# Kernel optimization log

Measured on AMD Instinct MI355X. Metric: run time of the kernel, lower is better.

## Reference

```python
import jax, jax.numpy as jnp
import numpy as np

B, N, D, H, L = 2, 2048, 128, 8, 3
V = 32          # NUM_ATOM_TYPES (assumed)
DH = D // H
SCALE = 1.0 / (DH ** 0.5)
NEG = -1e9      # stands in for -inf in the additive attention mask
EPS = 1e-5


def _ln(x, g, b):
    m = x.mean(-1, keepdims=True)
    v = ((x - m) ** 2).mean(-1, keepdims=True)
    return (x - m) / jnp.sqrt(v + EPS) * g + b


def setup_inputs() -> dict:
    key = jax.random.key(0)
    ks = jax.random.split(key, 24)
    nrm = lambda k, shape, std=0.02: jax.random.normal(k, shape, jnp.float32) * std
    atom_embed = nrm(ks[0], (V, D)).at[0].set(0.0)  # padding_idx = 0
    cons_embed = nrm(ks[1], (1, 1, D))
    in_w = nrm(ks[2], (D, D)); in_b = jnp.zeros((D,), jnp.float32)
    qkv_w = nrm(ks[3], (L, 3 * D, D)); qkv_b = jnp.zeros((L, 3 * D), jnp.float32)
    out_w = nrm(ks[4], (L, D, D)); out_b = jnp.zeros((L, D), jnp.float32)
    ln1_g = jnp.ones((L, D), jnp.float32); ln1_b = jnp.zeros((L, D), jnp.float32)
    ln2_g = jnp.ones((L, D), jnp.float32); ln2_b = jnp.zeros((L, D), jnp.float32)
    ff1_w = nrm(ks[5], (L, 4 * D, D)); ff1_b = jnp.zeros((L, 4 * D), jnp.float32)
    ff2_w = nrm(ks[6], (L, D, 4 * D)); ff2_b = jnp.zeros((L, D), jnp.float32)
    struct_bias = nrm(ks[7], (L,), 0.5)  # scalar per layer (init 0 in torch; randomized to exercise the path)
    head_ln_g = jnp.ones((D,), jnp.float32); head_ln_b = jnp.zeros((D,), jnp.float32)
    head_w = nrm(ks[8], (1, D)); head_b = jnp.zeros((1,), jnp.float32)
    is_atom = jax.random.bernoulli(ks[9], 0.5, (B, N))
    atom_id = jax.random.randint(ks[10], (B, N), 0, V)
    mask = jax.random.bernoulli(ks[11], 0.9, (B, N))
    adjacency = (jax.random.uniform(ks[12], (B, N, N)) < 0.002).astype(jnp.float32)
    adjacency = jnp.maximum(adjacency, jnp.eye(N, dtype=jnp.float32)[None])  # self-loops
    root_idx = jax.random.randint(ks[13], (B,), 0, N)
    return dict(atom_embed=atom_embed, cons_embed=cons_embed, in_w=in_w, in_b=in_b,
                qkv_w=qkv_w, qkv_b=qkv_b, out_w=out_w, out_b=out_b,
                ln1_g=ln1_g, ln1_b=ln1_b, ln2_g=ln2_g, ln2_b=ln2_b,
                ff1_w=ff1_w, ff1_b=ff1_b, ff2_w=ff2_w, ff2_b=ff2_b,
                struct_bias=struct_bias, head_ln_g=head_ln_g, head_ln_b=head_ln_b,
                head_w=head_w, head_b=head_b, adjacency=adjacency,
                is_atom=is_atom, atom_id=atom_id, mask=mask, root_idx=root_idx)


def reference(atom_embed, cons_embed, in_w, in_b, qkv_w, qkv_b, out_w, out_b,
              ln1_g, ln1_b, ln2_g, ln2_b, ff1_w, ff1_b, ff2_w, ff2_b,
              struct_bias, head_ln_g, head_ln_b, head_w, head_b,
              adjacency, is_atom, atom_id, mask, root_idx):
    # node embeddings
    ae = atom_embed[jnp.clip(atom_id, 0, V - 1)]                     # [B,N,D]
    h = jnp.where(is_atom[..., None], ae, jnp.broadcast_to(cons_embed, (B, N, D)))
    h = h @ in_w.T + in_b
    # additive attention mask: valid pairs OK; invalid query rows attend only to self
    pair_ok = mask[:, :, None] & mask[:, None, :]
    eye = jnp.eye(N, dtype=bool)[None]
    ok = pair_ok | ((~mask)[:, :, None] & eye)
    am = jnp.where(ok, 0.0, NEG).astype(jnp.float32)                 # [B,N,N]
    for i in range(L):
        x = _ln(h, ln1_g[i], ln1_b[i])
        qkv = (x @ qkv_w[i].T + qkv_b[i]).reshape(B, N, 3, H, DH)
        q, k, v = (jnp.transpose(qkv[:, :, j], (0, 2, 1, 3)) for j in range(3))  # [B,H,N,DH]
        scores = jnp.einsum('bhqd,bhkd->bhqk', q, k) * SCALE \
                 + struct_bias[i] * adjacency[:, None] + am[:, None]
        attn = jax.nn.softmax(scores, axis=-1)
        o = jnp.einsum('bhqk,bhkd->bhqd', attn, v)
        o = jnp.transpose(o, (0, 2, 1, 3)).reshape(B, N, D)
        h = h + (o @ out_w[i].T + out_b[i])
        x2 = _ln(h, ln2_g[i], ln2_b[i])
        f = jax.nn.gelu(x2 @ ff1_w[i].T + ff1_b[i], approximate=False)
        h = h + (f @ ff2_w[i].T + ff2_b[i])
    pooled = h[jnp.arange(B), root_idx]                              # [B,D]
    p = _ln(pooled, head_ln_g, head_ln_b)
    return (p @ head_w.T + head_b)[:, 0]                             # [B]
```

## Files before the change

kernel.cpp:

```cpp
#include <hip/hip_runtime.h>
#include <cmath>

#define NB 2
#define NN 2048
#define ND 128
#define NH 8
#define NL 3
#define NV 32
#define NDH 16
#define LN_EPS 1e-5f
#define QSCALE 0.36067376022224085f

typedef __bf16 bf8_t __attribute__((ext_vector_type(8)));
typedef __bf16 bf4_t __attribute__((ext_vector_type(4)));
typedef float f4x __attribute__((ext_vector_type(4)));
typedef float f16x __attribute__((ext_vector_type(16)));

struct CastArgs {
  const float* s[5];
  __bf16* d[5];
  int startblk[5];
};
__global__ __launch_bounds__(256) void prep_kernel(
    CastArgs a, const float* __restrict__ adj, unsigned long long* __restrict__ abits,
    const int* __restrict__ mask, unsigned long long* __restrict__ mbits) {
  int blk = blockIdx.x;
  int lane = threadIdx.x & 63;
  if (blk < 592) {
    int seg = 0;
#pragma unroll
    for (int i = 1; i < 5; i++) seg += (blk >= a.startblk[i]) ? 1 : 0;
    int i4 = (blk - a.startblk[seg]) * 256 + threadIdx.x;
    float4 v = ((const float4*)a.s[seg])[i4];
    bf4_t p = {(__bf16)v.x, (__bf16)v.y, (__bf16)v.z, (__bf16)v.w};
    ((bf4_t*)a.d[seg])[i4] = p;
  } else if (blk < 592 + 8192) {
    int g = ((blk - 592) * 4 + (threadIdx.x >> 6)) * 4;
    const float* p = adj + (size_t)g * 64 + lane;
    unsigned long long w0 = __ballot(p[0] != 0.0f);
    unsigned long long w1 = __ballot(p[64] != 0.0f);
    unsigned long long w2 = __ballot(p[128] != 0.0f);
    unsigned long long w3 = __ballot(p[192] != 0.0f);
    if (lane == 0) {
      abits[g] = w0; abits[g + 1] = w1; abits[g + 2] = w2; abits[g + 3] = w3;
    }
  } else {
    int g = (blk - 8784) * 4 + (threadIdx.x >> 6);
    int v = mask[g * 64 + lane];
    unsigned long long bal = __ballot(v != 0);
    if (lane == 0) mbits[g] = bal;
  }
}

template <int IN, int OUT2>
__global__ __launch_bounds__(512) void fused_kernel(
    const __bf16* __restrict__ Xb,
    const float* __restrict__ atom_embed, const float* __restrict__ cons_embed,
    const int* __restrict__ is_atom, const int* __restrict__ atom_id,
    const __bf16* __restrict__ W1, const float* __restrict__ b1,
    const float* __restrict__ Hin, float* __restrict__ Hout,
    const float* __restrict__ lng, const float* __restrict__ lnb,
    const __bf16* __restrict__ W2, const float* __restrict__ b2,
    __bf16* __restrict__ Fb,
    __bf16* __restrict__ Qb, __bf16* __restrict__ Kb, __bf16* __restrict__ Vt,
    const int* __restrict__ root_idx, const float* __restrict__ hg,
    const float* __restrict__ hbt, const float* __restrict__ hwp,
    const float* __restrict__ hbp, float* __restrict__ outp) {
  constexpr int K1 = (IN == 2) ? 512 : 128;
  constexpr int NK1 = K1 / 128;
  __shared__ __bf16 Xs[16][K1 + 8];
  __shared__ __bf16 Ws[128][136];
  __shared__ float Hs[16][132];
  __shared__ __bf16 X2[16][136];
  int m0 = blockIdx.x * 16;
  int g = blockIdx.y;
  int t = threadIdx.x;
  int lane = t & 63, w = t >> 6;
  int l15 = lane & 15, quad = lane >> 4;
  const int NC2 = (OUT2 == 1) ? 2 : (OUT2 == 2 ? (g == 0 ? 2 : 1) : 0);
  const int T = NK1 + NC2;

  if constexpr (IN == 0) {
    int r = t >> 5, c = t & 31;
    int row = m0 + r;
    int id = atom_id[row];
    id = id < 0 ? 0 : (id > NV - 1 ? NV - 1 : id);
    const float* src = is_atom[row] ? (atom_embed + (size_t)id * ND) : cons_embed;
    float4 v = *(const float4*)&src[c * 4];
    bf4_t p = {(__bf16)v.x, (__bf16)v.y, (__bf16)v.z, (__bf16)v.w};
    *(bf4_t*)&Xs[r][c * 4] = p;
  } else if constexpr (IN == 1) {
    int r = t >> 5, c = t & 31;
    *(bf4_t*)&Xs[r][c * 4] = *(const bf4_t*)&Xb[(size_t)(m0 + r) * 128 + c * 4];
  } else {
#pragma unroll
    for (int c = t; c < 1024; c += 512) {
      int r = c >> 6, ch = c & 63;
      *(bf8_t*)&Xs[r][ch * 8] = *(const bf8_t*)&Xb[(size_t)(m0 + r) * 512 + ch * 8];
    }
  }

  bf8_t wreg[4];
  auto issue = [&](int i) {
    const __bf16* base;
    int stride, rowoff, coloff;
    if (i < NK1) {
      base = W1; stride = K1; rowoff = 0; coloff = i * 128;
    } else {
      int j = i - NK1;
      int nc = (OUT2 == 1) ? (2 * g + j) : (g == 0 ? j : 2);
      base = W2; stride = 128; rowoff = nc * 128; coloff = 0;
    }
#pragma unroll
    for (int jj = 0; jj < 4; jj++) {
      int c = t + jj * 512;
      int r = c >> 4, ch = c & 15;
      wreg[jj] = *(const bf8_t*)&base[(size_t)(rowoff + r) * stride + coloff + ch * 8];
    }
  };
  issue(0);

  f4x acc = {0.f, 0.f, 0.f, 0.f};
  for (int i = 0; i < T; i++) {
    if (i) __syncthreads();
#pragma unroll
    for (int jj = 0; jj < 4; jj++) {
      int c = t + jj * 512;
      *(bf8_t*)&Ws[c >> 4][(c & 15) * 8] = wreg[jj];
    }
    __syncthreads();
    if (i + 1 < T) issue(i + 1);
    if (i < NK1) {
#pragma unroll
      for (int kk = 0; kk < 4; kk++) {
        bf8_t a = *(const bf8_t*)&Xs[l15][i * 128 + kk * 32 + quad * 8];
        bf8_t b = *(const bf8_t*)&Ws[w * 16 + l15][kk * 32 + quad * 8];
        acc = __builtin_amdgcn_mfma_f32_16x16x32_bf16(a, b, acc, 0, 0, 0);
      }
      if (i == NK1 - 1) {
        int n = w * 16 + l15;
        float bv = b1[n];
#pragma unroll
        for (int r = 0; r < 4; r++) {
          int m = quad * 4 + r;
          float v = acc[r] + bv;
          if constexpr (IN != 0) v += Hin[(size_t)(m0 + m) * ND + n];
          if (g == 0) Hout[(size_t)(m0 + m) * ND + n] = v;
          Hs[m][n] = v;
        }
        __syncthreads();
        if constexpr (OUT2 != 0) {
          int r = t >> 5, c = t & 31;
          float4 v = *(const float4*)&Hs[r][c * 4];
          float s1 = v.x + v.y + v.z + v.w;
          float s2 = v.x * v.x + v.y * v.y + v.z * v.z + v.w * v.w;
#pragma unroll
          for (int m = 16; m >= 1; m >>= 1) {
            s1 += __shfl_xor(s1, m, 64);
            s2 += __shfl_xor(s2, m, 64);
          }
          float mean = s1 * (1.0f / ND);
          float var = s2 * (1.0f / ND) - mean * mean;
          float rstd = rsqrtf(var + LN_EPS);
          float4 gg = *(const float4*)&lng[c * 4];
          float4 bb = *(const float4*)&lnb[c * 4];
          bf4_t p;
          p[0] = (__bf16)((v.x - mean) * rstd * gg.x + bb.x);
          p[1] = (__bf16)((v.y - mean) * rstd * gg.y + bb.y);
          p[2] = (__bf16)((v.z - mean) * rstd * gg.z + bb.z);
          p[3] = (__bf16)((v.w - mean) * rstd * gg.w + bb.w);
          *(bf4_t*)&X2[r][c * 4] = p;
        }
      }
    } else {
      int j = i - NK1;
      int nc = (OUT2 == 1) ? (2 * g + j) : (g == 0 ? j : 2);
      f4x a2 = {0.f, 0.f, 0.f, 0.f};
#pragma unroll
      for (int kk = 0; kk < 4; kk++) {
        bf8_t a = *(const bf8_t*)&X2[l15][kk * 32 + quad * 8];
        bf8_t b = *(const bf8_t*)&Ws[w * 16 + l15][kk * 32 + quad * 8];
        a2 = __builtin_amdgcn_mfma_f32_16x16x32_bf16(a, b, a2, 0, 0, 0);
      }
      int n = nc * 128 + w * 16 + l15;
      float bv = b2[n];
#pragma unroll
      for (int r = 0; r < 4; r++) {
        int m = m0 + quad * 4 + r;
        float v = a2[r] + bv;
        if constexpr (OUT2 == 1) {
          v = 0.5f * v * (1.0f + erff(v * 0.70710678118f));
          Fb[(size_t)m * 512 + n] = (__bf16)v;
        } else {
          if (n < ND) Qb[(size_t)m * ND + n] = (__bf16)(v * QSCALE);
          else if (n < 2 * ND) Kb[(size_t)m * ND + n - ND] = (__bf16)v;
          else {
            int c2 = n - 2 * ND, hh = c2 >> 4, d0 = c2 & 15;
            int bb2 = m >> 11, nn = m & 2047;
            Vt[((size_t)((bb2 * NH + hh) * NDH + d0)) * NN + nn] = (__bf16)v;
          }
        }
      }
    }
  }

  if constexpr (OUT2 == 0) {
    if (w < NB) {
      int rt = root_idx[w];
      int rglob = w * NN + rt;
      if (rglob >= m0 && rglob < m0 + 16) {
        int r = rglob - m0;
        float v0 = Hs[r][2 * lane], v1 = Hs[r][2 * lane + 1];
        float s1 = v0 + v1, s2 = v0 * v0 + v1 * v1;
#pragma unroll
        for (int m = 32; m >= 1; m >>= 1) {
          s1 += __shfl_xor(s1, m, 64);
          s2 += __shfl_xor(s2, m, 64);
        }
        float mean = s1 * (1.0f / ND);
        float var = s2 * (1.0f / ND) - mean * mean;
        float rstd = rsqrtf(var + LN_EPS);
        float p0 = (v0 - mean) * rstd * hg[2 * lane] + hbt[2 * lane];
        float p1 = (v1 - mean) * rstd * hg[2 * lane + 1] + hbt[2 * lane + 1];
        float part = p0 * hwp[2 * lane] + p1 * hwp[2 * lane + 1];
#pragma unroll
        for (int m = 32; m >= 1; m >>= 1) part += __shfl_xor(part, m, 64);
        if (lane == 0) outp[w] = part + hbp[0];
      }
    }
  }
}

__global__ __launch_bounds__(512) void attn_kernel(
    const __bf16* __restrict__ Qb, const __bf16* __restrict__ Kb,
    const __bf16* __restrict__ Vt, const unsigned int* __restrict__ adjbits,
    const unsigned int* __restrict__ maskbits, const int* __restrict__ mask,
    const float* __restrict__ sbias, int layer, __bf16* __restrict__ o) {
  int b = blockIdx.z, hh = blockIdx.y, q0 = blockIdx.x * 32;
  int wave = threadIdx.x >> 6;
  int lane = threadIdx.x & 63;
  int l31 = lane & 31, hi = lane >> 5;
  int l15 = lane & 15, quad = lane >> 4;
  float esb = __expf(sbias[layer]);
  const int bN = b * NN;
  const int kw0 = wave * 256;

  __shared__ __bf16 Pbuf[8][32][40];
  __shared__ float Ored[8][32][17];
  __shared__ float Lred[8][32];

  bf8_t Qf = *(const bf8_t*)(Qb + (size_t)(bN + q0 + l31) * ND + hh * NDH + hi * 8);

  int q = q0 + l31;
  int mq = mask[bN + q];
  const unsigned int* adjp = adjbits + (size_t)(bN + q) * (NN / 32) + (kw0 >> 5);
  const unsigned int* mbp = maskbits + (bN + kw0) / 32;
  const __bf16* kp = Kb + (size_t)(bN + kw0 + l31) * ND + hh * NDH + hi * 8;
  const __bf16* vp = Vt + (size_t)((b * NH + hh) * NDH + l15) * NN + kw0 + quad * 8;

  int dq = q - kw0;
  int tsel = dq >> 5;
  unsigned int selfw = 1u << (dq & 31);
  int sh4 = hi * 4;

  f4x Olo = {0.f, 0.f, 0.f, 0.f}, Ohi = {0.f, 0.f, 0.f, 0.f};
  float ls = 0.f;

  bf8_t Kf = *(const bf8_t*)kp;
  bf8_t Vf = *(const bf8_t*)vp;
  unsigned int aw = adjp[0];
  unsigned int mkw = mbp[0];

  for (int t = 0; t < 8; t++) {
    bf8_t Kn = Kf, Vn = Vf;
    unsigned int awn = aw, mkn = mkw;
    if (t < 7) {
      kp += 32 * ND;
      Kn = *(const bf8_t*)kp;
      Vn = *(const bf8_t*)(vp + (t + 1) * 32);
      awn = adjp[t + 1];
      mkn = mbp[t + 1];
    }
    f16x S = {0.f, 0.f, 0.f, 0.f, 0.f, 0.f, 0.f, 0.f,
              0.f, 0.f, 0.f, 0.f, 0.f, 0.f, 0.f, 0.f};
    S = __builtin_amdgcn_mfma_f32_32x32x16_bf16(Kf, Qf, S, 0, 0, 0);
    unsigned int okw = mq ? mkw : ((t == tsel) ? selfw : 0u);
    unsigned int wa = (aw & okw) >> sh4;
    unsigned int okh = okw >> sh4;
#pragma unroll
    for (int gg = 0; gg < 4; gg++) {
      bf4_t pk;
#pragma unroll
      for (int r = 0; r < 4; r++) {
        int c = gg * 8 + r;
        float e = __builtin_amdgcn_exp2f(S[gg * 4 + r]);
        float wgt = ((wa >> c) & 1) ? esb : (((okh >> c) & 1) ? 1.0f : 0.0f);
        float p = e * wgt;
        ls += p;
        pk[r] = (__bf16)p;
      }
      *(bf4_t*)&Pbuf[wave][l31][sh4 + gg * 8] = pk;
    }
    asm volatile("s_waitcnt lgkmcnt(0)" ::: "memory");
    bf8_t Plo = *(const bf8_t*)&Pbuf[wave][l15][quad * 8];
    bf8_t Phi = *(const bf8_t*)&Pbuf[wave][16 + l15][quad * 8];
    Olo = __builtin_amdgcn_mfma_f32_16x16x32_bf16(Plo, Vf, Olo, 0, 0, 0);
    Ohi = __builtin_amdgcn_mfma_f32_16x16x32_bf16(Phi, Vf, Ohi, 0, 0, 0);
    Kf = Kn; Vf = Vn; aw = awn; mkw = mkn;
  }

  ls += __shfl_xor(ls, 32, 64);
  if (hi == 0) Lred[wave][l31] = ls;
#pragma unroll
  for (int r = 0; r < 4; r++) {
    Ored[wave][quad * 4 + r][l15] = Olo[r];
    Ored[wave][16 + quad * 4 + r][l15] = Ohi[r];
  }
  __syncthreads();
  int row = threadIdx.x >> 4, col = threadIdx.x & 15;
  float s = 0.f, L = 0.f;
#pragma unroll
  for (int p = 0; p < 8; p++) {
    s += Ored[p][row][col];
    L += Lred[p][row];
  }
  o[(size_t)(bN + q0 + row) * ND + hh * NDH + col] = (__bf16)(s / L);
}

extern "C" void kernel_launch(void* const* d_in, const int* in_sizes, int n_in,
                              void* d_out, int out_size, void* d_ws, size_t ws_size,
                              hipStream_t stream) {
  const float* atom_embed = (const float*)d_in[0];
  const float* cons_embed = (const float*)d_in[1];
  const float* in_w  = (const float*)d_in[2];
  const float* in_b  = (const float*)d_in[3];
  const float* qkv_w = (const float*)d_in[4];
  const float* qkv_b = (const float*)d_in[5];
  const float* out_w = (const float*)d_in[6];
  const float* out_b = (const float*)d_in[7];
  const float* ln1_g = (const float*)d_in[8];
  const float* ln1_b = (const float*)d_in[9];
  const float* ln2_g = (const float*)d_in[10];
  const float* ln2_b = (const float*)d_in[11];
  const float* ff1_w = (const float*)d_in[12];
  const float* ff1_b = (const float*)d_in[13];
  const float* ff2_w = (const float*)d_in[14];
  const float* ff2_b = (const float*)d_in[15];
  const float* sbias = (const float*)d_in[16];
  const float* hg    = (const float*)d_in[17];
  const float* hbt   = (const float*)d_in[18];
  const float* hw    = (const float*)d_in[19];
  const float* hb    = (const float*)d_in[20];
  const float* adj   = (const float*)d_in[21];
  const int* is_atom = (const int*)d_in[22];
  const int* atom_id = (const int*)d_in[23];
  const int* mask    = (const int*)d_in[24];
  const int* root_idx= (const int*)d_in[25];
  float* out = (float*)d_out;

  const int MR = NB * NN;
  float* hA = (float*)d_ws;
  float* hB = hA + MR * ND;
  __bf16* fb   = (__bf16*)(hB + MR * ND);
  __bf16* Qb   = fb + MR * 512;
  __bf16* Kb   = Qb + MR * ND;
  __bf16* Vt   = Kb + MR * ND;
  __bf16* wbin = Vt + MR * ND;
  __bf16* wbqkv= wbin + ND * ND;
  __bf16* wbout= wbqkv + NL * 384 * ND;
  __bf16* wbff1= wbout + NL * ND * ND;
  __bf16* wbff2= wbff1 + NL * 512 * ND;
  unsigned int* adjb = (unsigned int*)(wbff2 + NL * ND * 512);
  unsigned int* mskb = adjb + NB * NN * NN / 32;
  __bf16* ob = (__bf16*)(mskb + 128);

  CastArgs ca;
  ca.s[0] = in_w;  ca.d[0] = wbin;  ca.startblk[0] = 0;
  ca.s[1] = qkv_w; ca.d[1] = wbqkv; ca.startblk[1] = 16;
  ca.s[2] = out_w; ca.d[2] = wbout; ca.startblk[2] = 160;
  ca.s[3] = ff1_w; ca.d[3] = wbff1; ca.startblk[3] = 208;
  ca.s[4] = ff2_w; ca.d[4] = wbff2; ca.startblk[4] = 400;
  prep_kernel<<<8800, 256, 0, stream>>>(ca, adj, (unsigned long long*)adjb,
                                        mask, (unsigned long long*)mskb);

  fused_kernel<0, 2><<<dim3(MR / 16, 2), 512, 0, stream>>>(
      nullptr, atom_embed, cons_embed, is_atom, atom_id,
      wbin, in_b, nullptr, hA, ln1_g, ln1_b,
      wbqkv, qkv_b, nullptr, Qb, Kb, Vt,
      nullptr, nullptr, nullptr, nullptr, nullptr, nullptr);

  for (int i = 0; i < NL; i++) {
    attn_kernel<<<dim3(NN / 32, NH, NB), 512, 0, stream>>>(
        Qb, Kb, Vt, adjb, mskb, mask, sbias, i, ob);
    fused_kernel<1, 1><<<dim3(MR / 16, 2), 512, 0, stream>>>(
        ob, nullptr, nullptr, nullptr, nullptr,
        wbout + (size_t)i * ND * ND, out_b + i * ND, hA, hB,
        ln2_g + i * ND, ln2_b + i * ND,
        wbff1 + (size_t)i * 512 * ND, ff1_b + i * 512, fb,
        nullptr, nullptr, nullptr,
        nullptr, nullptr, nullptr, nullptr, nullptr, nullptr);
    if (i < NL - 1) {
      fused_kernel<2, 2><<<dim3(MR / 16, 2), 512, 0, stream>>>(
          fb, nullptr, nullptr, nullptr, nullptr,
          wbff2 + (size_t)i * ND * 512, ff2_b + i * ND, hB, hA,
          ln1_g + (i + 1) * ND, ln1_b + (i + 1) * ND,
          wbqkv + (size_t)(i + 1) * 384 * ND, qkv_b + (i + 1) * 384, nullptr,
          Qb, Kb, Vt,
          nullptr, nullptr, nullptr, nullptr, nullptr, nullptr);
    } else {
      fused_kernel<2, 0><<<dim3(MR / 16, 1), 512, 0, stream>>>(
          fb, nullptr, nullptr, nullptr, nullptr,
          wbff2 + (size_t)i * ND * 512, ff2_b + i * ND, hB, hA,
          nullptr, nullptr, nullptr, nullptr, nullptr,
          nullptr, nullptr, nullptr,
          root_idx, hg, hbt, hw, hb, out);
    }
  }
}
```

Baseline: 264.8 us.

## Fuse out-proj, LN2, MLP and next-layer QKV into one per-layer kernel

Replaces the two per-layer GEMM kernels with a single layer kernel. It runs the output projection, LN2, FF1 with GELU, FF2 with residual, LN1 and the next layer's QKV projection in sequence, keeping the FF1 activations in shared memory. This drops the global round trip of the 4096x512 bf16 FFN buffer and one kernel launch per layer. In exchange, both y-blocks now redundantly compute the full out-proj and MLP, where FF1 columns used to be split between them. The per-block serial chain of weight-tile steps also gets longer.

Result: no change. 261.6 us (median of 2 runs) (-1.2%).

```diff
diff --git a/kernel.cpp b/kernel.cpp
--- a/kernel.cpp
+++ b/kernel.cpp
@@ -52,23 +52,15 @@
   }
 }
 
-template <int IN, int OUT2>
-__global__ __launch_bounds__(512) void fused_kernel(
-    const __bf16* __restrict__ Xb,
+__global__ __launch_bounds__(512) void fused0_kernel(
     const float* __restrict__ atom_embed, const float* __restrict__ cons_embed,
     const int* __restrict__ is_atom, const int* __restrict__ atom_id,
     const __bf16* __restrict__ W1, const float* __restrict__ b1,
-    const float* __restrict__ Hin, float* __restrict__ Hout,
+    float* __restrict__ Hout,
     const float* __restrict__ lng, const float* __restrict__ lnb,
     const __bf16* __restrict__ W2, const float* __restrict__ b2,
-    __bf16* __restrict__ Fb,
-    __bf16* __restrict__ Qb, __bf16* __restrict__ Kb, __bf16* __restrict__ Vt,
-    const int* __restrict__ root_idx, const float* __restrict__ hg,
-    const float* __restrict__ hbt, const float* __restrict__ hwp,
-    const float* __restrict__ hbp, float* __restrict__ outp) {
-  constexpr int K1 = (IN == 2) ? 512 : 128;
-  constexpr int NK1 = K1 / 128;
-  __shared__ __bf16 Xs[16][K1 + 8];
+    __bf16* __restrict__ Qb, __bf16* __restrict__ Kb, __bf16* __restrict__ Vt) {
+  __shared__ __bf16 Xs[16][136];
   __shared__ __bf16 Ws[128][136];
   __shared__ float Hs[16][132];
   __shared__ __bf16 X2[16][136];
@@ -77,10 +69,10 @@
   int t = threadIdx.x;
   int lane = t & 63, w = t >> 6;
   int l15 = lane & 15, quad = lane >> 4;
-  const int NC2 = (OUT2 == 1) ? 2 : (OUT2 == 2 ? (g == 0 ? 2 : 1) : 0);
-  const int T = NK1 + NC2;
-
-  if constexpr (IN == 0) {
+  const int NC2 = (g == 0) ? 2 : 1;
+  const int T = 1 + NC2;
+
+  {
     int r = t >> 5, c = t & 31;
     int row = m0 + r;
     int id = atom_id[row];
@@ -89,38 +81,174 @@
     float4 v = *(const float4*)&src[c * 4];
     bf4_t p = {(__bf16)v.x, (__bf16)v.y, (__bf16)v.z, (__bf16)v.w};
     *(bf4_t*)&Xs[r][c * 4] = p;
-  } else if constexpr (IN == 1) {
+  }
+
+  bf8_t wreg[4];
+  auto issue = [&](int i) {
+    const __bf16* base;
+    int rowoff;
+    if (i == 0) { base = W1; rowoff = 0; }
+    else {
+      int nc = (g == 0) ? (i - 1) : 2;
+      base = W2; rowoff = nc * 128;
+    }
+#pragma unroll
+    for (int jj = 0; jj < 4; jj++) {
+      int c = t + jj * 512;
+      wreg[jj] = *(const bf8_t*)&base[(size_t)(rowoff + (c >> 4)) * 128 + (c & 15) * 8];
+    }
+  };
+  issue(0);
+
+  for (int i = 0; i < T; i++) {
+    if (i) __syncthreads();
+#pragma unroll
+    for (int jj = 0; jj < 4; jj++) {
+      int c = t + jj * 512;
+      *(bf8_t*)&Ws[c >> 4][(c & 15) * 8] = wreg[jj];
+    }
+    __syncthreads();
+    if (i + 1 < T) issue(i + 1);
+    if (i == 0) {
+      f4x a1 = {0.f, 0.f, 0.f, 0.f};
+#pragma unroll
+      for (int kk = 0; kk < 4; kk++) {
+        bf8_t a = *(const bf8_t*)&Xs[l15][kk * 32 + quad * 8];
+        bf8_t b = *(const bf8_t*)&Ws[w * 16 + l15][kk * 32 + quad * 8];
+        a1 = __builtin_amdgcn_mfma_f32_16x16x32_bf16(a, b, a1, 0, 0, 0);
+      }
+      int n = w * 16 + l15;
+      float bv = b1[n];
+#pragma unroll
+      for (int r = 0; r < 4; r++) {
+        int m = quad * 4 + r;
+        float v = a1[r] + bv;
+        if (g == 0) Hout[(size_t)(m0 + m) * ND + n] = v;
+        Hs[m][n] = v;
+      }
+      __syncthreads();
+      {
+        int r = t >> 5, c = t & 31;
+        float4 v = *(const float4*)&Hs[r][c * 4];
+        float s1 = v.x + v.y + v.z + v.w;
+        float s2 = v.x * v.x + v.y * v.y + v.z * v.z + v.w * v.w;
+#pragma unroll
+        for (int m = 16; m >= 1; m >>= 1) {
+          s1 += __shfl_xor(s1, m, 64);
+          s2 += __shfl_xor(s2, m, 64);
+        }
+        float mean = s1 * (1.0f / ND);
+        float var = s2 * (1.0f / ND) - mean * mean;
+        float rstd = rsqrtf(var + LN_EPS);
+        float4 gg = *(const float4*)&lng[c * 4];
+        float4 bb = *(const float4*)&lnb[c * 4];
+        bf4_t p;
+        p[0] = (__bf16)((v.x - mean) * rstd * gg.x + bb.x);
+        p[1] = (__bf16)((v.y - mean) * rstd * gg.y + bb.y);
+        p[2] = (__bf16)((v.z - mean) * rstd * gg.z + bb.z);
+        p[3] = (__bf16)((v.w - mean) * rstd * gg.w + bb.w);
+        *(bf4_t*)&X2[r][c * 4] = p;
+      }
+    } else {
+      int nc = (g == 0) ? (i - 1) : 2;
+      f4x a2 = {0.f, 0.f, 0.f, 0.f};
+#pragma unroll
+      for (int kk = 0; kk < 4; kk++) {
+        bf8_t a = *(const bf8_t*)&X2[l15][kk * 32 + quad * 8];
+        bf8_t b = *(const bf8_t*)&Ws[w * 16 + l15][kk * 32 + quad * 8];
+        a2 = __builtin_amdgcn_mfma_f32_16x16x32_bf16(a, b, a2, 0, 0, 0);
+      }
+      int n = nc * 128 + w * 16 + l15;
+      float bv = b2[n];
+#pragma unroll
+      for (int r = 0; r < 4; r++) {
+        int m = m0 + quad * 4 + r;
+        float v = a2[r] + bv;
+        if (n < ND) Qb[(size_t)m * ND + n] = (__bf16)(v * QSCALE);
+        else if (n < 2 * ND) Kb[(size_t)m * ND + n - ND] = (__bf16)v;
+        else {
+          int c2 = n - 2 * ND, hh = c2 >> 4, d0 = c2 & 15;
+          int bb2 = m >> 11, nn = m & 2047;
+          Vt[((size_t)((bb2 * NH + hh) * NDH + d0)) * NN + nn] = (__bf16)v;
+        }
+      }
+    }
+  }
+}
+
+template <int LAST>
+__global__ __launch_bounds__(512) void layer_kernel(
+    const __bf16* __restrict__ Ob,
+    const __bf16* __restrict__ Wout, const float* __restrict__ bout,
+    const float* __restrict__ Hin, float* __restrict__ Hout,
+    const float* __restrict__ ln2g, const float* __restrict__ ln2b,
+    const __bf16* __restrict__ Wff1, const float* __restrict__ bff1,
+    const __bf16* __restrict__ Wff2, const float* __restrict__ bff2,
+    const float* __restrict__ ln1g, const float* __restrict__ ln1b,
+    const __bf16* __restrict__ Wqkv, const float* __restrict__ bqkv,
+    __bf16* __restrict__ Qb, __bf16* __restrict__ Kb, __bf16* __restrict__ Vt,
+    const int* __restrict__ root_idx, const float* __restrict__ hg,
+    const float* __restrict__ hbt, const float* __restrict__ hwp,
+    const float* __restrict__ hbp, float* __restrict__ outp) {
+  __shared__ __bf16 Xs[16][136];
+  __shared__ __bf16 Ws[128][136];
+  __shared__ float Hs[16][132];
+  __shared__ __bf16 X2[16][136];
+  __shared__ __bf16 Fs[16][520];
+  int m0 = blockIdx.x * 16;
+  int g = blockIdx.y;
+  int t = threadIdx.x;
+  int lane = t & 63, w = t >> 6;
+  int l15 = lane & 15, quad = lane >> 4;
+  const int NQ = LAST ? 0 : (g == 0 ? 2 : 1);
+  const int T = 9 + NQ;
+
+  {
     int r = t >> 5, c = t & 31;
-    *(bf4_t*)&Xs[r][c * 4] = *(const bf4_t*)&Xb[(size_t)(m0 + r) * 128 + c * 4];
-  } else {
-#pragma unroll
-    for (int c = t; c < 1024; c += 512) {
-      int r = c >> 6, ch = c & 63;
-      *(bf8_t*)&Xs[r][ch * 8] = *(const bf8_t*)&Xb[(size_t)(m0 + r) * 512 + ch * 8];
-    }
+    *(bf4_t*)&Xs[r][c * 4] = *(const bf4_t*)&Ob[(size_t)(m0 + r) * ND + c * 4];
   }
 
   bf8_t wreg[4];
   auto issue = [&](int i) {
     const __bf16* base;
     int stride, rowoff, coloff;
-    if (i < NK1) {
-      base = W1; stride = K1; rowoff = 0; coloff = i * 128;
-    } else {
-      int j = i - NK1;
-      int nc = (OUT2 == 1) ? (2 * g + j) : (g == 0 ? j : 2);
-      base = W2; stride = 128; rowoff = nc * 128; coloff = 0;
-    }
+    if (i == 0)     { base = Wout; stride = 128; rowoff = 0;             coloff = 0; }
+    else if (i < 5) { base = Wff1; stride = 128; rowoff = (i - 1) * 128; coloff = 0; }
+    else if (i < 9) { base = Wff2; stride = 512; rowoff = 0;             coloff = (i - 5) * 128; }
+    else            { int nc = (g == 0) ? (i - 9) : 2;
+                      base = Wqkv; stride = 128; rowoff = nc * 128;      coloff = 0; }
 #pragma unroll
     for (int jj = 0; jj < 4; jj++) {
       int c = t + jj * 512;
-      int r = c >> 4, ch = c & 15;
-      wreg[jj] = *(const bf8_t*)&base[(size_t)(rowoff + r) * stride + coloff + ch * 8];
+      wreg[jj] = *(const bf8_t*)&base[(size_t)(rowoff + (c >> 4)) * stride + coloff + (c & 15) * 8];
     }
   };
   issue(0);
 
-  f4x acc = {0.f, 0.f, 0.f, 0.f};
+  auto do_ln = [&](const float* g_, const float* b_) {
+    int r = t >> 5, c = t & 31;
+    float4 v = *(const float4*)&Hs[r][c * 4];
+    float s1 = v.x + v.y + v.z + v.w;
+    float s2 = v.x * v.x + v.y * v.y + v.z * v.z + v.w * v.w;
+#pragma unroll
+    for (int m = 16; m >= 1; m >>= 1) {
+      s1 += __shfl_xor(s1, m, 64);
+      s2 += __shfl_xor(s2, m, 64);
+    }
+    float mean = s1 * (1.0f / ND);
+    float var = s2 * (1.0f / ND) - mean * mean;
+    float rstd = rsqrtf(var + LN_EPS);
+    float4 gg = *(const float4*)&g_[c * 4];
+    float4 bb = *(const float4*)&b_[c * 4];
+    bf4_t p;
+    p[0] = (__bf16)((v.x - mean) * rstd * gg.x + bb.x);
+    p[1] = (__bf16)((v.y - mean) * rstd * gg.y + bb.y);
+    p[2] = (__bf16)((v.z - mean) * rstd * gg.z + bb.z);
+    p[3] = (__bf16)((v.w - mean) * rstd * gg.w + bb.w);
+    *(bf4_t*)&X2[r][c * 4] = p;
+  };
+
+  f4x acc2 = {0.f, 0.f, 0.f, 0.f};
   for (int i = 0; i < T; i++) {
     if (i) __syncthreads();
 #pragma unroll
@@ -130,51 +258,63 @@
     }
     __syncthreads();
     if (i + 1 < T) issue(i + 1);
-    if (i < NK1) {
+    if (i == 0) {
+      f4x a1 = {0.f, 0.f, 0.f, 0.f};
 #pragma unroll
       for (int kk = 0; kk < 4; kk++) {
-        bf8_t a = *(const bf8_t*)&Xs[l15][i * 128 + kk * 32 + quad * 8];
+        bf8_t a = *(const bf8_t*)&Xs[l15][kk * 32 + quad * 8];
         bf8_t b = *(const bf8_t*)&Ws[w * 16 + l15][kk * 32 + quad * 8];
-        acc = __builtin_amdgcn_mfma_f32_16x16x32_bf16(a, b, acc, 0, 0, 0);
-      }
-      if (i == NK1 - 1) {
+        a1 = __builtin_amdgcn_mfma_f32_16x16x32_bf16(a, b, a1, 0, 0, 0);
+      }
+      int n = w * 16 + l15;
+      float bv = bout[n];
+#pragma unroll
+      for (int r = 0; r < 4; r++) {
+        int m = quad * 4 + r;
+        Hs[m][n] = a1[r] + bv + Hin[(size_t)(m0 + m) * ND + n];
+      }
+      __syncthreads();
+      do_ln(ln2g, ln2b);
+    } else if (i < 5) {
+      int c = i - 1;
+      f4x a1 = {0.f, 0.f, 0.f, 0.f};
+#pragma unroll
+      for (int kk = 0; kk < 4; kk++) {
+        bf8_t a = *(const bf8_t*)&X2[l15][kk * 32 + quad * 8];
+        bf8_t b = *(const bf8_t*)&Ws[w * 16 + l15][kk * 32 + quad * 8];
+        a1 = __builtin_amdgcn_mfma_f32_16x16x32_bf16(a, b, a1, 0, 0, 0);
+      }
+      int n = w * 16 + l15;
+      float bv = bff1[c * 128 + n];
+#pragma unroll
+      for (int r = 0; r < 4; r++) {
+        float v = a1[r] + bv;
+        v = 0.5f * v * (1.0f + erff(v * 0.70710678118f));
+        Fs[quad * 4 + r][c * 128 + n] = (__bf16)v;
+      }
+    } else if (i < 9) {
+      int j = i - 5;
+#pragma unroll
+      for (int kk = 0; kk < 4; kk++) {
+        bf8_t a = *(const bf8_t*)&Fs[l15][j * 128 + kk * 32 + quad * 8];
+        bf8_t b = *(const bf8_t*)&Ws[w * 16 + l15][kk * 32 + quad * 8];
+        acc2 = __builtin_amdgcn_mfma_f32_16x16x32_bf16(a, b, acc2, 0, 0, 0);
+      }
+      if (j == 3) {
         int n = w * 16 + l15;
-        float bv = b1[n];
+        float bv = bff2[n];
 #pragma unroll
         for (int r = 0; r < 4; r++) {
           int m = quad * 4 + r;
-          float v = acc[r] + bv;
-          if constexpr (IN != 0) v += Hin[(size_t)(m0 + m) * ND + n];
+          float v = acc2[r] + bv + Hs[m][n];
+          Hs[m][n] = v;
           if (g == 0) Hout[(size_t)(m0 + m) * ND + n] = v;
-          Hs[m][n] = v;
         }
         __syncthreads();
-        if constexpr (OUT2 != 0) {
-          int r = t >> 5, c = t & 31;
-          float4 v = *(const float4*)&Hs[r][c * 4];
-          float s1 = v.x + v.y + v.z + v.w;
-          float s2 = v.x * v.x + v.y * v.y + v.z * v.z + v.w * v.w;
-#pragma unroll
-          for (int m = 16; m >= 1; m >>= 1) {
-            s1 += __shfl_xor(s1, m, 64);
-            s2 += __shfl_xor(s2, m, 64);
-          }
-          float mean = s1 * (1.0f / ND);
-          float var = s2 * (1.0f / ND) - mean * mean;
-          float rstd = rsqrtf(var + LN_EPS);
-          float4 gg = *(const float4*)&lng[c * 4];
-          float4 bb = *(const float4*)&lnb[c * 4];
-          bf4_t p;
-          p[0] = (__bf16)((v.x - mean) * rstd * gg.x + bb.x);
-          p[1] = (__bf16)((v.y - mean) * rstd * gg.y + bb.y);
-          p[2] = (__bf16)((v.z - mean) * rstd * gg.z + bb.z);
-          p[3] = (__bf16)((v.w - mean) * rstd * gg.w + bb.w);
-          *(bf4_t*)&X2[r][c * 4] = p;
-        }
+        if constexpr (!LAST) do_ln(ln1g, ln1b);
       }
     } else {
-      int j = i - NK1;
-      int nc = (OUT2 == 1) ? (2 * g + j) : (g == 0 ? j : 2);
+      int nc = (g == 0) ? (i - 9) : 2;
       f4x a2 = {0.f, 0.f, 0.f, 0.f};
 #pragma unroll
       for (int kk = 0; kk < 4; kk++) {
@@ -183,28 +323,23 @@
         a2 = __builtin_amdgcn_mfma_f32_16x16x32_bf16(a, b, a2, 0, 0, 0);
       }
       int n = nc * 128 + w * 16 + l15;
-      float bv = b2[n];
+      float bv = bqkv[n];
 #pragma unroll
       for (int r = 0; r < 4; r++) {
         int m = m0 + quad * 4 + r;
         float v = a2[r] + bv;
-        if constexpr (OUT2 == 1) {
-          v = 0.5f * v * (1.0f + erff(v * 0.70710678118f));
-          Fb[(size_t)m * 512 + n] = (__bf16)v;
-        } else {
-          if (n < ND) Qb[(size_t)m * ND + n] = (__bf16)(v * QSCALE);
-          else if (n < 2 * ND) Kb[(size_t)m * ND + n - ND] = (__bf16)v;
-          else {
-            int c2 = n - 2 * ND, hh = c2 >> 4, d0 = c2 & 15;
-            int bb2 = m >> 11, nn = m & 2047;
-            Vt[((size_t)((bb2 * NH + hh) * NDH + d0)) * NN + nn] = (__bf16)v;
-          }
+        if (n < ND) Qb[(size_t)m * ND + n] = (__bf16)(v * QSCALE);
+        else if (n < 2 * ND) Kb[(size_t)m * ND + n - ND] = (__bf16)v;
+        else {
+          int c2 = n - 2 * ND, hh = c2 >> 4, d0 = c2 & 15;
+          int bb2 = m >> 11, nn = m & 2047;
+          Vt[((size_t)((bb2 * NH + hh) * NDH + d0)) * NN + nn] = (__bf16)v;
         }
       }
     }
   }
 
-  if constexpr (OUT2 == 0) {
+  if constexpr (LAST) {
     if (w < NB) {
       int rt = root_idx[w];
       int rglob = w * NN + rt;
@@ -361,8 +496,7 @@
   const int MR = NB * NN;
   float* hA = (float*)d_ws;
   float* hB = hA + MR * ND;
-  __bf16* fb   = (__bf16*)(hB + MR * ND);
-  __bf16* Qb   = fb + MR * 512;
+  __bf16* Qb   = (__bf16*)(hB + MR * ND);
   __bf16* Kb   = Qb + MR * ND;
   __bf16* Vt   = Kb + MR * ND;
   __bf16* wbin = Vt + MR * ND;
@@ -383,35 +517,32 @@
   prep_kernel<<<8800, 256, 0, stream>>>(ca, adj, (unsigned long long*)adjb,
                                         mask, (unsigned long long*)mskb);
 
-  fused_kernel<0, 2><<<dim3(MR / 16, 2), 512, 0, stream>>>(
-      nullptr, atom_embed, cons_embed, is_atom, atom_id,
-      wbin, in_b, nullptr, hA, ln1_g, ln1_b,
-      wbqkv, qkv_b, nullptr, Qb, Kb, Vt,
-      nullptr, nullptr, nullptr, nullptr, nullptr, nullptr);
-
+  fused0_kernel<<<dim3(MR / 16, 2), 512, 0, stream>>>(
+      atom_embed, cons_embed, is_atom, atom_id,
+      wbin, in_b, hA, ln1_g, ln1_b, wbqkv, qkv_b, Qb, Kb, Vt);
+
+  const float* hin[3]  = {hA, hB, hA};
+  float* hout[3]       = {hB, hA, hB};
   for (int i = 0; i < NL; i++) {
     attn_kernel<<<dim3(NN / 32, NH, NB), 512, 0, stream>>>(
         Qb, Kb, Vt, adjb, mskb, mask, sbias, i, ob);
-    fused_kernel<1, 1><<<dim3(MR / 16, 2), 512, 0, stream>>>(
-        ob, nullptr, nullptr, nullptr, nullptr,
-        wbout + (size_t)i * ND * ND, out_b + i * ND, hA, hB,
-        ln2_g + i * ND, ln2_b + i * ND,
-        wbff1 + (size_t)i * 512 * ND, ff1_b + i * 512, fb,
-        nullptr, nullptr, nullptr,
-        nullptr, nullptr, nullptr, nullptr, nullptr, nullptr);
     if (i < NL - 1) {
-      fused_kernel<2, 2><<<dim3(MR / 16, 2), 512, 0, stream>>>(
-          fb, nullptr, nullptr, nullptr, nullptr,
-          wbff2 + (size_t)i * ND * 512, ff2_b + i * ND, hB, hA,
+      layer_kernel<0><<<dim3(MR / 16, 2), 512, 0, stream>>>(
+          ob, wbout + (size_t)i * ND * ND, out_b + i * ND, hin[i], hout[i],
+          ln2_g + i * ND, ln2_b + i * ND,
+          wbff1 + (size_t)i * 512 * ND, ff1_b + i * 512,
+          wbff2 + (size_t)i * ND * 512, ff2_b + i * ND,
           ln1_g + (i + 1) * ND, ln1_b + (i + 1) * ND,
-          wbqkv + (size_t)(i + 1) * 384 * ND, qkv_b + (i + 1) * 384, nullptr,
+          wbqkv + (size_t)(i + 1) * 384 * ND, qkv_b + (i + 1) * 384,
           Qb, Kb, Vt,
           nullptr, nullptr, nullptr, nullptr, nullptr, nullptr);
     } else {
-      fused_kernel<2, 0><<<dim3(MR / 16, 1), 512, 0, stream>>>(
-          fb, nullptr, nullptr, nullptr, nullptr,
-          wbff2 + (size_t)i * ND * 512, ff2_b + i * ND, hB, hA,
-          nullptr, nullptr, nullptr, nullptr, nullptr,
+      layer_kernel<1><<<dim3(MR / 16, 1), 512, 0, stream>>>(
+          ob, wbout + (size_t)i * ND * ND, out_b + i * ND, hin[i], hout[i],
+          ln2_g + i * ND, ln2_b + i * ND,
+          wbff1 + (size_t)i * 512 * ND, ff1_b + i * 512,
+          wbff2 + (size_t)i * ND * 512, ff2_b + i * ND,
+          nullptr, nullptr, nullptr, nullptr,
           nullptr, nullptr, nullptr,
           root_idx, hg, hbt, hw, hb, out);
     }
```
